# Optimization experiments

Measured on AMD Instinct MI355X. Metric: run time of the kernel, lower is better.

The kernel has to match this reference:

```python
import jax, jax.numpy as jnp
import numpy as np


def setup_inputs() -> dict:
    key = jax.random.key(0)
    ks = jax.random.split(key, 8)
    B, T, S, E, H = 8, 1024, 1024, 768, 768
    scale = 1.0 / np.sqrt(E)
    return {
        "x": jax.random.normal(ks[0], (B, T, E), dtype=jnp.float32),
        "encoder_out": jax.random.normal(ks[1], (B, S, E), dtype=jnp.float32),
        "Wq": jax.random.normal(ks[2], (E, H), dtype=jnp.float32) * scale,
        "bq": jnp.zeros((H,), dtype=jnp.float32),
        "Wk": jax.random.normal(ks[3], (E, H), dtype=jnp.float32) * scale,
        "bk": jnp.zeros((H,), dtype=jnp.float32),
        "Wv": jax.random.normal(ks[4], (E, H), dtype=jnp.float32) * scale,
        "bv": jnp.zeros((H,), dtype=jnp.float32),
        "Wp": jax.random.normal(ks[5], (H, E), dtype=jnp.float32) * (1.0 / np.sqrt(H)),
        "bp": jnp.zeros((E,), dtype=jnp.float32),
    }


def reference(x, encoder_out, Wq, bq, Wk, bk, Wv, bv, Wp, bp):
    # Single-head cross-attention: q from x, k/v from encoder_out.
    q = x @ Wq + bq                    # [B,T,H]
    k = encoder_out @ Wk + bk          # [B,S,H]
    v = encoder_out @ Wv + bv          # [B,S,H]
    H = q.shape[-1]
    scores = jnp.einsum("bth,bsh->bts", q, k) * (H ** -0.5)  # [B,T,S]
    attn = jax.nn.softmax(scores, axis=-1)
    # dropout is identity in eval mode
    out = jnp.einsum("bts,bsh->bth", attn, v)                # [B,T,H]
    return out @ Wp + bp                                     # [B,T,E]
```

## Files before the change

kernel.cpp:

```cpp
#include <hip/hip_runtime.h>


typedef __bf16 bf16x8 __attribute__((ext_vector_type(8)));
typedef float  f32x4  __attribute__((ext_vector_type(4)));

#define WAIT_VM8 __builtin_amdgcn_s_waitcnt(0x0F78)
#define WAIT_VM0 __builtin_amdgcn_s_waitcnt(0x0F70)
#define BAR      __builtin_amdgcn_s_barrier()

__device__ __forceinline__ unsigned short f2bf(float f) {
    unsigned int u = __float_as_uint(f);
    u += 0x7fffu + ((u >> 16) & 1u);
    return (unsigned short)(u >> 16);
}

__device__ __forceinline__ void async_copy16(const void* g, void* s) {
    __builtin_amdgcn_global_load_lds(
        (const __attribute__((address_space(1))) void*)g,
        (__attribute__((address_space(3))) void*)s, 16, 0, 0);
}

__device__ __forceinline__ void gemm_core(
    const unsigned short* __restrict__ Ag,
    const unsigned short* __restrict__ Bg,
    const int K,
    float* __restrict__ Cf, unsigned short* __restrict__ Cb,
    const long ldc, const int transC, const float* __restrict__ bias,
    const float scale, const long row0, const long col0)
{
    __shared__ __align__(16) unsigned short As0[8192];
    __shared__ __align__(16) unsigned short As1[8192];
    __shared__ __align__(16) unsigned short Bs0[8192];
    __shared__ __align__(16) unsigned short Bs1[8192];

    const int tid  = threadIdx.x;
    const int lane = tid & 63;
    const int quad = lane >> 4;
    const int l16  = lane & 15;
    const int wv   = tid >> 6;
    const int wm   = (wv >> 1) * 64;
    const int wn   = (wv & 1) * 64;

    const int j8 = ((lane & 7) ^ ((lane >> 3) & 7)) * 8;
    const int rb = wv * 32 + (lane >> 3);
    const unsigned short* sa_src = Ag + (long)rb * K + j8;
    const unsigned short* sb_src = Bg + (long)rb * K + j8;
    const int dbase = (wv * 256 + lane) * 8;

    f32x4 acc[4][4];
#pragma unroll
    for (int i = 0; i < 4; ++i)
#pragma unroll
        for (int j = 0; j < 4; ++j)
            acc[i][j] = f32x4{0.f, 0.f, 0.f, 0.f};

    auto stage = [&](unsigned short* dA, unsigned short* dB, int k0) {
#pragma unroll
        for (int h = 0; h < 4; ++h) {
            async_copy16(sa_src + (long)(h * 8) * K + k0, &dA[dbase + h * 512]);
            async_copy16(sb_src + (long)(h * 8) * K + k0, &dB[dbase + h * 512]);
        }
    };

    auto compute = [&](const unsigned short* sA, const unsigned short* sB) {
#pragma unroll
        for (int h = 0; h < 2; ++h) {
            bf16x8 af[4], bf[4];
            const int sl = ((quad + h * 4) ^ (l16 & 7)) * 8;
#pragma unroll
            for (int i = 0; i < 4; ++i) {
                af[i] = *(const bf16x8*)&sA[(wm + i * 16 + l16) * 64 + sl];
                bf[i] = *(const bf16x8*)&sB[(wn + i * 16 + l16) * 64 + sl];
            }
#pragma unroll
            for (int i = 0; i < 4; ++i)
#pragma unroll
                for (int j = 0; j < 4; ++j)
                    acc[i][j] = __builtin_amdgcn_mfma_f32_16x16x32_bf16(
                        af[i], bf[j], acc[i][j], 0, 0, 0);
        }
    };

    const int nk = K >> 6;
    stage(As0, Bs0, 0);
    stage(As1, Bs1, 64);
    int k0 = 128;

    for (int t = 0; t < nk - 2; t += 2) {
        WAIT_VM8; BAR;
        compute(As0, Bs0);
        BAR;
        stage(As0, Bs0, k0); k0 += 64;

        WAIT_VM8; BAR;
        compute(As1, Bs1);
        BAR;
        stage(As1, Bs1, k0); k0 += 64;
    }
    WAIT_VM8; BAR;
    compute(As0, Bs0);
    WAIT_VM0; BAR;
    compute(As1, Bs1);

#pragma unroll
    for (int i = 0; i < 4; ++i) {
#pragma unroll
        for (int j = 0; j < 4; ++j) {
            const long r0 = row0 + wm + i * 16 + quad * 4;
            const long c  = col0 + wn + j * 16 + l16;
            const float bb = bias ? bias[c] : 0.0f;
#pragma unroll
            for (int r = 0; r < 4; ++r) {
                const float v = acc[i][j][r] * scale + bb;
                const long rr = r0 + r;
                if (Cb) {
                    if (transC) {
                        Cb[((rr >> 10) * 768 + c) * 1024 + (rr & 1023)] = f2bf(v);
                    } else {
                        Cb[rr * ldc + c] = f2bf(v);
                    }
                } else {
                    Cf[rr * ldc + c] = v;
                }
            }
        }
    }
}


__global__ __launch_bounds__(256, 2) void proj_qkv(
    const unsigned short* __restrict__ xb, const unsigned short* __restrict__ eb,
    const unsigned short* __restrict__ wqt, const unsigned short* __restrict__ wkt,
    const unsigned short* __restrict__ wvt,
    const float* __restrict__ bq, const float* __restrict__ bk,
    const float* __restrict__ bv,
    unsigned short* __restrict__ q, unsigned short* __restrict__ k,
    unsigned short* __restrict__ vt)
{
    const unsigned short *A, *Bt; const float* bias; unsigned short* C;
    int trans = 0;
    switch (blockIdx.z) {
        case 0:  A = xb; Bt = wqt; bias = bq; C = q;  break;
        case 1:  A = eb; Bt = wkt; bias = bk; C = k;  break;
        default: A = eb; Bt = wvt; bias = bv; C = vt; trans = 1; break;
    }
    const long row0 = (long)blockIdx.x * 128;
    const long col0 = (long)blockIdx.y * 128;
    gemm_core(A + row0 * 768, Bt + col0 * 768, 768,
              nullptr, C, 768, trans, bias, 1.0f, row0, col0);
}

__global__ __launch_bounds__(256, 2) void scores_gemm(
    const unsigned short* __restrict__ q, const unsigned short* __restrict__ k,
    float* __restrict__ sc, float scale)
{
    const long b    = blockIdx.z;
    const long row0 = (long)blockIdx.x * 128;
    const long col0 = (long)blockIdx.y * 128;
    gemm_core(q + (b * 1024 + row0) * 768, k + b * 786432 + col0 * 768, 768,
              sc + b * 1048576, nullptr, 1024, 0, nullptr, scale, row0, col0);
}

__global__ __launch_bounds__(256, 2) void pv_gemm(
    const unsigned short* __restrict__ p, const unsigned short* __restrict__ vt,
    unsigned short* __restrict__ ao)
{
    const long b    = blockIdx.z;
    const long row0 = (long)blockIdx.x * 128;
    const long col0 = (long)blockIdx.y * 128;
    gemm_core(p + (b * 1024 + row0) * 1024, vt + b * 786432 + col0 * 1024, 1024,
              nullptr, ao + b * 786432, 768, 0, nullptr, 1.0f, row0, col0);
}

__global__ __launch_bounds__(256, 2) void outproj_gemm(
    const unsigned short* __restrict__ ao, const unsigned short* __restrict__ wpt,
    float* __restrict__ out, const float* __restrict__ bp)
{
    const long row0 = (long)blockIdx.x * 128;
    const long col0 = (long)blockIdx.y * 128;
    gemm_core(ao + row0 * 768, wpt + col0 * 768, 768,
              out, nullptr, 768, 0, bp, 1.0f, row0, col0);
}


__global__ __launch_bounds__(256) void convert_inputs(
    const float* __restrict__ x, const float* __restrict__ enc,
    unsigned short* __restrict__ xb, unsigned short* __restrict__ eb, int nper)
{
    const int i = blockIdx.x * 256 + threadIdx.x;
    const bool second = (i >= nper);
    const int idx = second ? i - nper : i;
    const float4 v = second ? ((const float4*)enc)[idx] : ((const float4*)x)[idx];
    ushort4 o;
    o.x = f2bf(v.x); o.y = f2bf(v.y); o.z = f2bf(v.z); o.w = f2bf(v.w);
    if (second) ((ushort4*)eb)[idx] = o;
    else        ((ushort4*)xb)[idx] = o;
}

__global__ __launch_bounds__(256) void transpose_w(
    const float* __restrict__ w0, const float* __restrict__ w1,
    const float* __restrict__ w2, const float* __restrict__ w3,
    unsigned short* __restrict__ o0, unsigned short* __restrict__ o1,
    unsigned short* __restrict__ o2, unsigned short* __restrict__ o3)
{
    const float* w; unsigned short* o;
    switch (blockIdx.z) {
        case 0:  w = w0; o = o0; break;
        case 1:  w = w1; o = o1; break;
        case 2:  w = w2; o = o2; break;
        default: w = w3; o = o3; break;
    }
    __shared__ float t[32][33];
    const int tx = threadIdx.x & 31;
    const int ty = threadIdx.x >> 5;
    const int k0 = blockIdx.x * 32;
    const int n0 = blockIdx.y * 32;
#pragma unroll
    for (int i = 0; i < 4; ++i)
        t[ty + i * 8][tx] = w[(long)(k0 + ty + i * 8) * 768 + n0 + tx];
    __syncthreads();
#pragma unroll
    for (int i = 0; i < 4; ++i)
        o[(long)(n0 + ty + i * 8) * 768 + k0 + tx] = f2bf(t[tx][ty + i * 8]);
}

__global__ __launch_bounds__(256) void softmax_rows(
    const float* __restrict__ S, unsigned short* __restrict__ P)
{
    const long row = blockIdx.x;
    const float* s = S + row * 1024;
    unsigned short* p = P + row * 1024;
    const int tid  = threadIdx.x;
    const int lane = tid & 63;
    const int wave = tid >> 6;

    float4 v = ((const float4*)s)[tid];
    float m = fmaxf(fmaxf(v.x, v.y), fmaxf(v.z, v.w));
#pragma unroll
    for (int off = 32; off > 0; off >>= 1)
        m = fmaxf(m, __shfl_xor(m, off));
    __shared__ float redm[4], reds[4];
    if (lane == 0) redm[wave] = m;
    __syncthreads();
    m = fmaxf(fmaxf(redm[0], redm[1]), fmaxf(redm[2], redm[3]));

    const float e0 = __expf(v.x - m), e1 = __expf(v.y - m);
    const float e2 = __expf(v.z - m), e3 = __expf(v.w - m);
    float sum = e0 + e1 + e2 + e3;
#pragma unroll
    for (int off = 32; off > 0; off >>= 1)
        sum += __shfl_xor(sum, off);
    if (lane == 0) reds[wave] = sum;
    __syncthreads();
    const float inv = 1.0f / (reds[0] + reds[1] + reds[2] + reds[3]);

    ushort4 o;
    o.x = f2bf(e0 * inv); o.y = f2bf(e1 * inv);
    o.z = f2bf(e2 * inv); o.w = f2bf(e3 * inv);
    ((ushort4*)p)[tid] = o;
}


extern "C" void kernel_launch(void* const* d_in, const int* in_sizes, int n_in,
                              void* d_out, int out_size, void* d_ws, size_t ws_size,
                              hipStream_t stream) {
    const float* x   = (const float*)d_in[0];
    const float* enc = (const float*)d_in[1];
    const float* Wq  = (const float*)d_in[2];
    const float* bq  = (const float*)d_in[3];
    const float* Wk  = (const float*)d_in[4];
    const float* bk  = (const float*)d_in[5];
    const float* Wv  = (const float*)d_in[6];
    const float* bv  = (const float*)d_in[7];
    const float* Wp  = (const float*)d_in[8];
    const float* bp  = (const float*)d_in[9];
    float* out = (float*)d_out;

    char* ws = (char*)d_ws;
    unsigned short* xb  = (unsigned short*)(ws + 0);
    unsigned short* eb  = (unsigned short*)(ws + 12582912);
    unsigned short* q   = (unsigned short*)(ws + 25165824);
    unsigned short* k   = (unsigned short*)(ws + 37748736);
    unsigned short* vt  = (unsigned short*)(ws + 50331648);
    unsigned short* wqt = (unsigned short*)(ws + 62914560);
    unsigned short* wkt = (unsigned short*)(ws + 64094208);
    unsigned short* wvt = (unsigned short*)(ws + 65273856);
    unsigned short* wpt = (unsigned short*)(ws + 66453504);
    float*          sc  = (float*)(ws + 67633152);
    unsigned short* p   = (unsigned short*)(ws + 0);
    unsigned short* ao  = (unsigned short*)(ws + 67633152);

    const float scale = 0.03608439182435161f;

    convert_inputs<<<12288, 256, 0, stream>>>(x, enc, xb, eb, 1572864);

    transpose_w<<<dim3(24, 24, 4), 256, 0, stream>>>(Wq, Wk, Wv, Wp, wqt, wkt, wvt, wpt);

    proj_qkv<<<dim3(64, 6, 3), 256, 0, stream>>>(xb, eb, wqt, wkt, wvt, bq, bk, bv, q, k, vt);

    scores_gemm<<<dim3(8, 8, 8), 256, 0, stream>>>(q, k, sc, scale);

    softmax_rows<<<8192, 256, 0, stream>>>(sc, p);

    pv_gemm<<<dim3(8, 6, 8), 256, 0, stream>>>(p, vt, ao);

    outproj_gemm<<<dim3(64, 6, 1), 256, 0, stream>>>(ao, wpt, out, bp);
}
```

Before: 238.3 us.

## Enlarge GEMM tiles to 256x128 with 512-thread blocks and split prefetch

The shared GEMM core moves from 128x128 tiles with 256 threads to 256x128 tiles with 512 threads (8 waves). The A tile in LDS doubles in size. The K-loop is restructured so the next tile's loads are issued in chunks interleaved with compute, with a finer vmcnt wait and s_setprio around MFMA bursts. This is meant to improve B-operand reuse and overlap loads with MFMA work. In exchange it halves grid size (e.g. scores 256 blocks) and raises LDS use per block, which may reduce occupancy and CU fill.

Result: slower. 253.1 us (+6.2%).

```diff
diff --git a/kernel.cpp b/kernel.cpp
--- a/kernel.cpp
+++ b/kernel.cpp
@@ -4,7 +4,7 @@
 typedef __bf16 bf16x8 __attribute__((ext_vector_type(8)));
 typedef float  f32x4  __attribute__((ext_vector_type(4)));
 
-#define WAIT_VM8 __builtin_amdgcn_s_waitcnt(0x0F78)
+#define WAIT_VM2 __builtin_amdgcn_s_waitcnt(0x0F72)
 #define WAIT_VM0 __builtin_amdgcn_s_waitcnt(0x0F70)
 #define BAR      __builtin_amdgcn_s_barrier()
 
@@ -28,8 +28,8 @@
     const long ldc, const int transC, const float* __restrict__ bias,
     const float scale, const long row0, const long col0)
 {
-    __shared__ __align__(16) unsigned short As0[8192];
-    __shared__ __align__(16) unsigned short As1[8192];
+    __shared__ __align__(16) unsigned short As0[16384];
+    __shared__ __align__(16) unsigned short As1[16384];
     __shared__ __align__(16) unsigned short Bs0[8192];
     __shared__ __align__(16) unsigned short Bs1[8192];
 
@@ -41,11 +41,10 @@
     const int wm   = (wv >> 1) * 64;
     const int wn   = (wv & 1) * 64;
 
-    const int j8 = ((lane & 7) ^ ((lane >> 3) & 7)) * 8;
-    const int rb = wv * 32 + (lane >> 3);
-    const unsigned short* sa_src = Ag + (long)rb * K + j8;
-    const unsigned short* sb_src = Bg + (long)rb * K + j8;
-    const int dbase = (wv * 256 + lane) * 8;
+    const int ksw = ((tid & 7) ^ ((tid >> 3) & 7)) * 8;
+    const unsigned short* a_src = Ag + (long)(tid >> 3) * K + ksw;
+    const unsigned short* b_src = Bg + (long)(tid >> 3) * K + ksw;
+    const int dofs = tid * 8;
 
     f32x4 acc[4][4];
 #pragma unroll
@@ -54,53 +53,60 @@
         for (int j = 0; j < 4; ++j)
             acc[i][j] = f32x4{0.f, 0.f, 0.f, 0.f};
 
-    auto stage = [&](unsigned short* dA, unsigned short* dB, int k0) {
-#pragma unroll
-        for (int h = 0; h < 4; ++h) {
-            async_copy16(sa_src + (long)(h * 8) * K + k0, &dA[dbase + h * 512]);
-            async_copy16(sb_src + (long)(h * 8) * K + k0, &dB[dbase + h * 512]);
+    auto stA = [&](unsigned short* dA, int h, int kk) {
+        async_copy16(a_src + (long)(h * 64) * K + kk, &dA[h * 4096 + dofs]);
+    };
+    auto stB = [&](unsigned short* dB, int h, int kk) {
+        async_copy16(b_src + (long)(h * 64) * K + kk, &dB[h * 4096 + dofs]);
+    };
+
+    auto do_quad = [&](const unsigned short* sA, const unsigned short* sB,
+                       int mh, int nh) {
+        bf16x8 af[2][2], bfr[2][2];
+#pragma unroll
+        for (int ks = 0; ks < 2; ++ks) {
+            const int sl = ((quad + ks * 4) ^ (l16 & 7)) * 8;
+#pragma unroll
+            for (int i = 0; i < 2; ++i) {
+                af[i][ks]  = *(const bf16x8*)&sA[(wm + (mh * 2 + i) * 16 + l16) * 64 + sl];
+                bfr[i][ks] = *(const bf16x8*)&sB[(wn + (nh * 2 + i) * 16 + l16) * 64 + sl];
+            }
         }
+        __builtin_amdgcn_s_setprio(1);
+#pragma unroll
+        for (int ks = 0; ks < 2; ++ks)
+#pragma unroll
+            for (int i = 0; i < 2; ++i)
+#pragma unroll
+                for (int j = 0; j < 2; ++j)
+                    acc[mh * 2 + i][nh * 2 + j] = __builtin_amdgcn_mfma_f32_16x16x32_bf16(
+                        af[i][ks], bfr[j][ks], acc[mh * 2 + i][nh * 2 + j], 0, 0, 0);
+        __builtin_amdgcn_s_setprio(0);
     };
 
-    auto compute = [&](const unsigned short* sA, const unsigned short* sB) {
-#pragma unroll
-        for (int h = 0; h < 2; ++h) {
-            bf16x8 af[4], bf[4];
-            const int sl = ((quad + h * 4) ^ (l16 & 7)) * 8;
-#pragma unroll
-            for (int i = 0; i < 4; ++i) {
-                af[i] = *(const bf16x8*)&sA[(wm + i * 16 + l16) * 64 + sl];
-                bf[i] = *(const bf16x8*)&sB[(wn + i * 16 + l16) * 64 + sl];
-            }
-#pragma unroll
-            for (int i = 0; i < 4; ++i)
-#pragma unroll
-                for (int j = 0; j < 4; ++j)
-                    acc[i][j] = __builtin_amdgcn_mfma_f32_16x16x32_bf16(
-                        af[i], bf[j], acc[i][j], 0, 0, 0);
-        }
+    auto tile_step = [&](const unsigned short* rA, const unsigned short* rB,
+                         unsigned short* wA, unsigned short* wB, int kk, bool last) {
+        BAR;
+        if (!last) { stA(wA, 0, kk); stB(wB, 0, kk); WAIT_VM2; }
+        else       { WAIT_VM0; }
+        BAR;
+        if (!last) { stA(wA, 1, kk); stB(wB, 1, kk); stA(wA, 2, kk); stA(wA, 3, kk); }
+        do_quad(rA, rB, 0, 0);
+        do_quad(rA, rB, 0, 1);
+        do_quad(rA, rB, 1, 0);
+        do_quad(rA, rB, 1, 1);
     };
 
-    const int nk = K >> 6;
-    stage(As0, Bs0, 0);
-    stage(As1, Bs1, 64);
-    int k0 = 128;
-
-    for (int t = 0; t < nk - 2; t += 2) {
-        WAIT_VM8; BAR;
-        compute(As0, Bs0);
-        BAR;
-        stage(As0, Bs0, k0); k0 += 64;
-
-        WAIT_VM8; BAR;
-        compute(As1, Bs1);
-        BAR;
-        stage(As1, Bs1, k0); k0 += 64;
+    const int nt = K >> 6;
+    stA(As0, 0, 0); stB(Bs0, 0, 0); stA(As0, 1, 0); stB(Bs0, 1, 0);
+    stA(As0, 2, 0); stA(As0, 3, 0);
+    int kk = 64;
+    for (int t = 0; t < nt - 2; t += 2) {
+        tile_step(As0, Bs0, As1, Bs1, kk, false); kk += 64;
+        tile_step(As1, Bs1, As0, Bs0, kk, false); kk += 64;
     }
-    WAIT_VM8; BAR;
-    compute(As0, Bs0);
-    WAIT_VM0; BAR;
-    compute(As1, Bs1);
+    tile_step(As0, Bs0, As1, Bs1, kk, false);
+    tile_step(As1, Bs1, As0, Bs0, 0, true);
 
 #pragma unroll
     for (int i = 0; i < 4; ++i) {
@@ -128,7 +134,7 @@
 }
 
 
-__global__ __launch_bounds__(256, 2) void proj_qkv(
+__global__ __launch_bounds__(512, 2) void proj_qkv(
     const unsigned short* __restrict__ xb, const unsigned short* __restrict__ eb,
     const unsigned short* __restrict__ wqt, const unsigned short* __restrict__ wkt,
     const unsigned short* __restrict__ wvt,
@@ -144,39 +150,39 @@
         case 1:  A = eb; Bt = wkt; bias = bk; C = k;  break;
         default: A = eb; Bt = wvt; bias = bv; C = vt; trans = 1; break;
     }
-    const long row0 = (long)blockIdx.x * 128;
+    const long row0 = (long)blockIdx.x * 256;
     const long col0 = (long)blockIdx.y * 128;
     gemm_core(A + row0 * 768, Bt + col0 * 768, 768,
               nullptr, C, 768, trans, bias, 1.0f, row0, col0);
 }
 
-__global__ __launch_bounds__(256, 2) void scores_gemm(
+__global__ __launch_bounds__(512, 2) void scores_gemm(
     const unsigned short* __restrict__ q, const unsigned short* __restrict__ k,
     float* __restrict__ sc, float scale)
 {
     const long b    = blockIdx.z;
-    const long row0 = (long)blockIdx.x * 128;
+    const long row0 = (long)blockIdx.x * 256;
     const long col0 = (long)blockIdx.y * 128;
     gemm_core(q + (b * 1024 + row0) * 768, k + b * 786432 + col0 * 768, 768,
               sc + b * 1048576, nullptr, 1024, 0, nullptr, scale, row0, col0);
 }
 
-__global__ __launch_bounds__(256, 2) void pv_gemm(
+__global__ __launch_bounds__(512, 2) void pv_gemm(
     const unsigned short* __restrict__ p, const unsigned short* __restrict__ vt,
     unsigned short* __restrict__ ao)
 {
     const long b    = blockIdx.z;
-    const long row0 = (long)blockIdx.x * 128;
+    const long row0 = (long)blockIdx.x * 256;
     const long col0 = (long)blockIdx.y * 128;
     gemm_core(p + (b * 1024 + row0) * 1024, vt + b * 786432 + col0 * 1024, 1024,
               nullptr, ao + b * 786432, 768, 0, nullptr, 1.0f, row0, col0);
 }
 
-__global__ __launch_bounds__(256, 2) void outproj_gemm(
+__global__ __launch_bounds__(512, 2) void outproj_gemm(
     const unsigned short* __restrict__ ao, const unsigned short* __restrict__ wpt,
     float* __restrict__ out, const float* __restrict__ bp)
 {
-    const long row0 = (long)blockIdx.x * 128;
+    const long row0 = (long)blockIdx.x * 256;
     const long col0 = (long)blockIdx.y * 128;
     gemm_core(ao + row0 * 768, wpt + col0 * 768, 768,
               out, nullptr, 768, 0, bp, 1.0f, row0, col0);
@@ -296,13 +302,13 @@
 
     transpose_w<<<dim3(24, 24, 4), 256, 0, stream>>>(Wq, Wk, Wv, Wp, wqt, wkt, wvt, wpt);
 
-    proj_qkv<<<dim3(64, 6, 3), 256, 0, stream>>>(xb, eb, wqt, wkt, wvt, bq, bk, bv, q, k, vt);
-
-    scores_gemm<<<dim3(8, 8, 8), 256, 0, stream>>>(q, k, sc, scale);
+    proj_qkv<<<dim3(32, 6, 3), 512, 0, stream>>>(xb, eb, wqt, wkt, wvt, bq, bk, bv, q, k, vt);
+
+    scores_gemm<<<dim3(4, 8, 8), 512, 0, stream>>>(q, k, sc, scale);
 
     softmax_rows<<<8192, 256, 0, stream>>>(sc, p);
 
-    pv_gemm<<<dim3(8, 6, 8), 256, 0, stream>>>(p, vt, ao);
-
-    outproj_gemm<<<dim3(64, 6, 1), 256, 0, stream>>>(ao, wpt, out, bp);
-}
+    pv_gemm<<<dim3(4, 6, 8), 512, 0, stream>>>(p, vt, ao);
+
+    outproj_gemm<<<dim3(32, 6, 1), 512, 0, stream>>>(ao, wpt, out, bp);
+}
```
